# Optimization experiments

Measured on AMD Instinct MI355X. Metric: run time of the kernel, lower is better.

## Reference

```python
import jax, jax.numpy as jnp
import numpy as np

N_NODES = 100000
N_EDGES = 1600000
IN_F, HID, OUT_F = 50, 256, 121


def setup_inputs() -> dict:
    key = jax.random.key(0)
    ks = jax.random.split(key, 8)
    x = jax.random.normal(ks[0], (N_NODES, IN_F), dtype=jnp.float32)
    edge_index = jax.random.randint(ks[1], (2, N_EDGES), 0, N_NODES, dtype=jnp.int64)
    W1 = jax.random.normal(ks[2], (IN_F, HID), dtype=jnp.float32) * (1.0 / np.sqrt(IN_F))
    b1 = jnp.zeros((HID,), dtype=jnp.float32)
    W2 = jax.random.normal(ks[3], (HID, HID), dtype=jnp.float32) * (1.0 / np.sqrt(HID))
    b2 = jnp.zeros((HID,), dtype=jnp.float32)
    W3 = jax.random.normal(ks[4], (HID, OUT_F), dtype=jnp.float32) * (1.0 / np.sqrt(HID))
    b3 = jnp.zeros((OUT_F,), dtype=jnp.float32)
    return {"x": x, "edge_index": edge_index, "W1": W1, "b1": b1,
            "W2": W2, "b2": b2, "W3": W3, "b3": b3}


def _gcn_norm(edge_index, num_nodes):
    # PyG gcn_norm: add self-loops, symmetric degree normalization.
    loop = jnp.arange(num_nodes, dtype=edge_index.dtype)
    row = jnp.concatenate([edge_index[0], loop])  # source
    col = jnp.concatenate([edge_index[1], loop])  # target (aggregation dim)
    ones = jnp.ones(row.shape[0], dtype=jnp.float32)
    deg = jax.ops.segment_sum(ones, col, num_segments=num_nodes)
    dinv = jnp.where(deg > 0, jax.lax.rsqrt(deg), 0.0)
    norm = dinv[row] * dinv[col]  # [E+N]
    return row, col, norm


def _gcn_conv(x, W, b, row, col, norm, num_nodes):
    h = x @ W                                   # [N, F_out] dense transform
    msg = h[row] * norm[:, None]                # gather + scale  [E+N, F_out]
    agg = jax.ops.segment_sum(msg, col, num_segments=num_nodes)  # scatter-add
    return agg + b


def reference(x, edge_index, W1, b1, W2, b2, W3, b3):
    n = x.shape[0]
    row, col, norm = _gcn_norm(edge_index, n)
    # layer 1 + relu (dropout is identity in eval mode)
    x1 = _gcn_conv(x, W1, b1, row, col, norm, n)
    h = jax.nn.relu(x1)
    # layer 2 + relu
    x1 = _gcn_conv(h, W2, b2, row, col, norm, n)
    h = jax.nn.relu(x1)
    # layer 3; module returns pre-relu output x1 of the last conv
    x1 = _gcn_conv(h, W3, b3, row, col, norm, n)
    return x1
```

## Files before the change

### kernel.cpp

```cpp
#include <hip/hip_runtime.h>


#define IN_F 50
#define HID  256
#define OUT_F 121
#define KP1  64
#define NP3  128
#define MPAD 100096

typedef __attribute__((ext_vector_type(8))) short bf16x8;
typedef __attribute__((ext_vector_type(4))) float f32x4;

__device__ __forceinline__ float bf2f(unsigned short u) {
    union { unsigned int i; float f; } x; x.i = ((unsigned int)u) << 16; return x.f;
}
__device__ __forceinline__ unsigned short f2bf(float f) {
    union { float f; unsigned int i; } x; x.f = f;
    unsigned int r = x.i + 0x7FFFu + ((x.i >> 16) & 1u);
    return (unsigned short)(r >> 16);
}

__device__ __forceinline__ void gl2lds16(const void* g, void* l) {
    __builtin_amdgcn_global_load_lds(
        (const __attribute__((address_space(1))) void*)g,
        (__attribute__((address_space(3))) void*)l, 16, 0, 0);
}

__global__ void k_detect(const int* __restrict__ ei, int* __restrict__ flag, int N) {
    int i = threadIdx.x;
    int lo = ei[2 * i], hi = ei[2 * i + 1];
    int bad = (hi != 0) || ((unsigned)lo >= (unsigned)N);
    unsigned long long m = __ballot(bad);
    if (threadIdx.x == 0) *flag = (m == 0ULL) ? 1 : 0;
}


__global__ void k_count(const int* __restrict__ ei, const int* __restrict__ flag,
                        int* __restrict__ cnt, int E, int N) {
    int t = blockIdx.x * blockDim.x + threadIdx.x;
    if (t >= E) return;
    int f = *flag;
    int c = f ? ei[2 * (E + t)] : ei[E + t];
    c = min(max(c, 0), N - 1);
    atomicAdd(&cnt[c], 1);
}

__global__ __launch_bounds__(1024) void k_scan(const int* __restrict__ cnt,
                                               int* __restrict__ offs,
                                               float* __restrict__ dinv, int n) {
    __shared__ int wsum[16];
    __shared__ int s_carry;
    int lane = threadIdx.x & 63, wid = threadIdx.x >> 6;
    if (threadIdx.x == 0) s_carry = 0;
    __syncthreads();
    for (int base = 0; base < n; base += 4096) {
        int i0 = base + (int)threadIdx.x * 4;
        int v0 = (i0 + 0 < n) ? cnt[i0 + 0] : 0;
        int v1 = (i0 + 1 < n) ? cnt[i0 + 1] : 0;
        int v2 = (i0 + 2 < n) ? cnt[i0 + 2] : 0;
        int v3 = (i0 + 3 < n) ? cnt[i0 + 3] : 0;
        int s1 = v0 + v1, s2 = s1 + v2, tsum = s2 + v3;
        int x = tsum;
        #pragma unroll
        for (int d = 1; d < 64; d <<= 1) {
            int y = __shfl_up(x, d, 64);
            if (lane >= d) x += y;
        }
        if (lane == 63) wsum[wid] = x;
        __syncthreads();
        int wpre = 0;
        #pragma unroll
        for (int j = 0; j < 16; j++) wpre += (j < wid) ? wsum[j] : 0;
        int carry = s_carry;
        int e0 = carry + wpre + x - tsum;
        if (i0 + 0 < n) { offs[i0+0]=e0;    dinv[i0+0]=rsqrtf((float)(v0+1)); }
        if (i0 + 1 < n) { offs[i0+1]=e0+v0; dinv[i0+1]=rsqrtf((float)(v1+1)); }
        if (i0 + 2 < n) { offs[i0+2]=e0+s1; dinv[i0+2]=rsqrtf((float)(v2+1)); }
        if (i0 + 3 < n) { offs[i0+3]=e0+s2; dinv[i0+3]=rsqrtf((float)(v3+1)); }
        __syncthreads();
        if (threadIdx.x == 1023) s_carry = carry + wpre + x;
        __syncthreads();
    }
    if (threadIdx.x == 0) offs[n] = s_carry;
}

__global__ void k_fill(const int* __restrict__ ei, const int* __restrict__ flag,
                       const int* __restrict__ offs,
                       int* __restrict__ fillc, int* __restrict__ rowidx, int E, int N) {
    int t = blockIdx.x * blockDim.x + threadIdx.x;
    if (t >= E) return;
    int f = *flag;
    int c = f ? ei[2 * (E + t)] : ei[E + t];
    int r = f ? ei[2 * t] : ei[t];
    c = min(max(c, 0), N - 1);
    r = min(max(r, 0), N - 1);
    int pos = offs[c] + atomicAdd(&fillc[c], 1);
    if ((unsigned)pos < (unsigned)E) rowidx[pos] = r;
}


__global__ void k_padx(const float* __restrict__ x, const float* __restrict__ dinv,
                       unsigned short* __restrict__ Xs, int N) {
    int idx = blockIdx.x * blockDim.x + threadIdx.x;
    if (idx >= N * KP1) return;
    int node = idx >> 6, k = idx & 63;
    Xs[idx] = (k < IN_F) ? f2bf(dinv[node] * x[node * IN_F + k]) : (unsigned short)0;
}

__global__ void k_tr(const float* __restrict__ W, unsigned short* __restrict__ Bt,
                     int K, int Nw, int Kp, int Np) {
    int idx = blockIdx.x * blockDim.x + threadIdx.x;
    if (idx >= Np * Kp) return;
    int nn = idx / Kp, k = idx - nn * Kp;
    Bt[idx] = (k < K && nn < Nw) ? f2bf(W[k * Nw + nn]) : (unsigned short)0;
}

__global__ __launch_bounds__(256) void k_gemm_lds(const unsigned short* __restrict__ A,
                                                  const unsigned short* __restrict__ Bt,
                                                  const float* __restrict__ dinv,
                                                  const float* __restrict__ bias,
                                                  unsigned short* __restrict__ C,
                                                  int K, int Nout,
                                                  int BIAS, int RELU, int SCALE) {
    __shared__ char lds[16384];
    const int tid = threadIdx.x;
    const int wid = tid >> 6, lane = tid & 63;
    const int wm = wid & 1, wn = wid >> 1;
    const int quad = lane >> 4, ml = lane & 15;
    const int m0 = blockIdx.x * 128;
    const int n0g = blockIdx.y * 128;

    f32x4 acc[4][4];
    #pragma unroll
    for (int a = 0; a < 4; a++)
        #pragma unroll
        for (int b = 0; b < 4; b++) acc[a][b] = (f32x4){0.f, 0.f, 0.f, 0.f};

    for (int kk = 0; kk < K; kk += 32) {
        #pragma unroll
        for (int r = 0; r < 2; r++) {
            int c = r * 256 + tid;
            int row = c >> 2, q = c & 3;
            gl2lds16(A  + (size_t)(m0  + row) * K + kk + q * 8, lds + c * 16);
            gl2lds16(Bt + (size_t)(n0g + row) * K + kk + q * 8, lds + 8192 + c * 16);
        }
        __syncthreads();
        bf16x8 af[4], bfv[4];
        #pragma unroll
        for (int mf = 0; mf < 4; mf++)
            af[mf] = *(const bf16x8*)(lds + ((wm * 64 + mf * 16 + ml) * 64 + quad * 16));
        #pragma unroll
        for (int nf = 0; nf < 4; nf++)
            bfv[nf] = *(const bf16x8*)(lds + 8192 + ((wn * 64 + nf * 16 + ml) * 64 + quad * 16));
        #pragma unroll
        for (int mf = 0; mf < 4; mf++)
            #pragma unroll
            for (int nf = 0; nf < 4; nf++)
                acc[mf][nf] = __builtin_amdgcn_mfma_f32_16x16x32_bf16(af[mf], bfv[nf], acc[mf][nf], 0, 0, 0);
        __syncthreads();
    }

    #pragma unroll
    for (int mf = 0; mf < 4; mf++) {
        int r0 = m0 + wm * 64 + mf * 16 + quad * 4;
        float dd[4] = {1.f, 1.f, 1.f, 1.f};
        if (SCALE) { dd[0]=dinv[r0]; dd[1]=dinv[r0+1]; dd[2]=dinv[r0+2]; dd[3]=dinv[r0+3]; }
        #pragma unroll
        for (int nf = 0; nf < 4; nf++) {
            int col = n0g + wn * 64 + nf * 16 + ml;
            float bb = BIAS ? bias[col] : 0.f;
            #pragma unroll
            for (int i = 0; i < 4; i++) {
                float v = acc[mf][nf][i] + bb;
                if (RELU) v = fmaxf(v, 0.f);
                v *= dd[i];
                C[(size_t)(r0 + i) * Nout + col] = f2bf(v);
            }
        }
    }
}


__device__ __forceinline__ int rclamp(int r, int N) { return min(max(r, 0), N - 1); }

__global__ void k_aggx(const unsigned short* __restrict__ Xs,
                       const int* __restrict__ offs, const int* __restrict__ rowidx,
                       const float* __restrict__ dinv, unsigned short* __restrict__ Y, int N) {
    int wid = threadIdx.x >> 6, lane = threadIdx.x & 63;
    int sub = lane >> 3, sl = lane & 7;
    int node = blockIdx.x * 32 + wid * 8 + sub;
    int nc = min(node, N - 1);
    int c = sl * 8;
    bf16x8 s = *(const bf16x8*)(Xs + (size_t)nc * KP1 + c);
    float a[8];
    #pragma unroll
    for (int k = 0; k < 8; k++) a[k] = bf2f((unsigned short)s[k]);
    int e = offs[nc], end = offs[nc + 1];
    if (node >= N) { e = 0; end = 0; }
    while (__any(e < end)) {
        int r[4]; float m[4];
        #pragma unroll
        for (int j = 0; j < 4; j++) {
            int idx = e + j;
            m[j] = (idx < end) ? 1.f : 0.f;
            idx = min(idx, end - 1); idx = max(idx, 0);
            r[j] = rclamp(rowidx[idx], N);
        }
        bf16x8 u[4];
        #pragma unroll
        for (int j = 0; j < 4; j++)
            u[j] = *(const bf16x8*)(Xs + (size_t)r[j] * KP1 + c);
        #pragma unroll
        for (int j = 0; j < 4; j++)
            #pragma unroll
            for (int k = 0; k < 8; k++)
                a[k] = fmaf(bf2f((unsigned short)u[j][k]), m[j], a[k]);
        e += 4;
    }
    if (node < N) {
        float dv = dinv[node];
        bf16x8 o;
        #pragma unroll
        for (int k = 0; k < 8; k++) o[k] = (short)f2bf(a[k] * dv);
        *(bf16x8*)(Y + (size_t)node * KP1 + c) = o;
    }
}

__global__ void k_agg256(const unsigned short* __restrict__ Hn,
                         const int* __restrict__ offs, const int* __restrict__ rowidx,
                         const float* __restrict__ dinv, unsigned short* __restrict__ Y, int N) {
    int wid = threadIdx.x >> 6, lane = threadIdx.x & 63;
    int sub = lane >> 5, sl = lane & 31;
    int node = blockIdx.x * 8 + wid * 2 + sub;
    int nc = min(node, N - 1);
    int c = sl * 8;
    bf16x8 s = *(const bf16x8*)(Hn + (size_t)nc * HID + c);
    float a[8];
    #pragma unroll
    for (int k = 0; k < 8; k++) a[k] = bf2f((unsigned short)s[k]);
    int e = offs[nc], end = offs[nc + 1];
    if (node >= N) { e = 0; end = 0; }
    while (__any(e < end)) {
        int r[4]; float m[4];
        #pragma unroll
        for (int j = 0; j < 4; j++) {
            int idx = e + j;
            m[j] = (idx < end) ? 1.f : 0.f;
            idx = min(idx, end - 1); idx = max(idx, 0);
            r[j] = rclamp(rowidx[idx], N);
        }
        bf16x8 u[4];
        #pragma unroll
        for (int j = 0; j < 4; j++)
            u[j] = *(const bf16x8*)(Hn + (size_t)r[j] * HID + c);
        #pragma unroll
        for (int j = 0; j < 4; j++)
            #pragma unroll
            for (int k = 0; k < 8; k++)
                a[k] = fmaf(bf2f((unsigned short)u[j][k]), m[j], a[k]);
        e += 4;
    }
    if (node < N) {
        float dv = dinv[node];
        bf16x8 o;
        #pragma unroll
        for (int k = 0; k < 8; k++) o[k] = (short)f2bf(a[k] * dv);
        *(bf16x8*)(Y + (size_t)node * HID + c) = o;
    }
}

__global__ void k_aggout(const unsigned short* __restrict__ G,
                         const int* __restrict__ offs, const int* __restrict__ rowidx,
                         const float* __restrict__ dinv, const float* __restrict__ bias,
                         float* __restrict__ out, int N) {
    int wid = threadIdx.x >> 6, lane = threadIdx.x & 63;
    int sub = lane >> 4, sl = lane & 15;
    int node = blockIdx.x * 16 + wid * 4 + sub;
    int nc = min(node, N - 1);
    int c = sl * 8;
    bf16x8 s = *(const bf16x8*)(G + (size_t)nc * NP3 + c);
    float a[8];
    #pragma unroll
    for (int k = 0; k < 8; k++) a[k] = bf2f((unsigned short)s[k]);
    int e = offs[nc], end = offs[nc + 1];
    if (node >= N) { e = 0; end = 0; }
    while (__any(e < end)) {
        int r[4]; float m[4];
        #pragma unroll
        for (int j = 0; j < 4; j++) {
            int idx = e + j;
            m[j] = (idx < end) ? 1.f : 0.f;
            idx = min(idx, end - 1); idx = max(idx, 0);
            r[j] = rclamp(rowidx[idx], N);
        }
        bf16x8 u[4];
        #pragma unroll
        for (int j = 0; j < 4; j++)
            u[j] = *(const bf16x8*)(G + (size_t)r[j] * NP3 + c);
        #pragma unroll
        for (int j = 0; j < 4; j++)
            #pragma unroll
            for (int k = 0; k < 8; k++)
                a[k] = fmaf(bf2f((unsigned short)u[j][k]), m[j], a[k]);
        e += 4;
    }
    if (node < N) {
        float dv = dinv[node];
        #pragma unroll
        for (int k = 0; k < 8; k++) {
            int col = c + k;
            if (col < OUT_F)
                out[(size_t)node * OUT_F + col] = fmaf(a[k], dv, bias[col]);
        }
    }
}


extern "C" void kernel_launch(void* const* d_in, const int* in_sizes, int n_in,
                              void* d_out, int out_size, void* d_ws, size_t ws_size,
                              hipStream_t stream) {
    const float* x  = (const float*)d_in[0];
    const int*   ei = (const int*)d_in[1];
    const float* W1 = (const float*)d_in[2];
    const float* b1 = (const float*)d_in[3];
    const float* W2 = (const float*)d_in[4];
    const float* b2 = (const float*)d_in[5];
    const float* W3 = (const float*)d_in[6];
    const float* b3 = (const float*)d_in[7];
    float* out = (float*)d_out;

    const int N = in_sizes[0] / IN_F;
    const int E = in_sizes[1] / 2;

    char* w = (char*)d_ws;
    size_t off = 0;
    auto alloc = [&](size_t bytes) -> char* {
        char* p = w + off;
        off += (bytes + 255) & ~(size_t)255;
        return p;
    };
    int*   cnt    = (int*)  alloc((size_t)N * 4);
    int*   offs   = (int*)  alloc((size_t)(N + 1) * 4);
    int*   fillc  = (int*)  alloc((size_t)N * 4);
    float* dinv   = (float*)alloc((size_t)MPAD * 4);
    int*   flag   = (int*)  alloc(256);
    int*   rowidx = (int*)  alloc((size_t)E * 4);
    unsigned short* Bt1 = (unsigned short*)alloc((size_t)HID * KP1 * 2);
    unsigned short* Bt2 = (unsigned short*)alloc((size_t)HID * HID * 2);
    unsigned short* Bt3 = (unsigned short*)alloc((size_t)NP3 * HID * 2);
    unsigned short* bufA = (unsigned short*)alloc((size_t)MPAD * HID * 2);
    unsigned short* bufB = (unsigned short*)alloc((size_t)MPAD * HID * 2);
    unsigned short* Xs  = bufA;
    unsigned short* Y1  = bufB;
    unsigned short* H1s = bufA;
    unsigned short* Y2  = bufB;
    unsigned short* H2  = bufA;
    unsigned short* G3  = bufB;

    hipMemsetAsync(cnt, 0, (size_t)N * 4, stream);
    hipMemsetAsync(fillc, 0, (size_t)N * 4, stream);
    hipMemsetAsync(rowidx, 0, (size_t)E * 4, stream);

    k_detect<<<1, 64, 0, stream>>>(ei, flag, N);
    k_count<<<(E + 255) / 256, 256, 0, stream>>>(ei, flag, cnt, E, N);
    k_scan<<<1, 1024, 0, stream>>>(cnt, offs, dinv, N);
    k_fill<<<(E + 255) / 256, 256, 0, stream>>>(ei, flag, offs, fillc, rowidx, E, N);

    k_padx<<<(N * KP1 + 255) / 256, 256, 0, stream>>>(x, dinv, Xs, N);
    k_tr<<<(HID * KP1 + 255) / 256, 256, 0, stream>>>(W1, Bt1, IN_F, HID, KP1, HID);
    k_tr<<<(HID * HID + 255) / 256, 256, 0, stream>>>(W2, Bt2, HID, HID, HID, HID);
    k_tr<<<(NP3 * HID + 255) / 256, 256, 0, stream>>>(W3, Bt3, HID, OUT_F, HID, NP3);

    dim3 g12(MPAD / 128, HID / 128);
    dim3 g3(MPAD / 128, NP3 / 128);

    k_aggx<<<(N + 31) / 32, 256, 0, stream>>>(Xs, offs, rowidx, dinv, Y1, N);
    k_gemm_lds<<<g12, 256, 0, stream>>>(Y1, Bt1, dinv, b1, H1s, KP1, HID, 1, 1, 1);
    k_agg256<<<(N + 7) / 8, 256, 0, stream>>>(H1s, offs, rowidx, dinv, Y2, N);
    k_gemm_lds<<<g12, 256, 0, stream>>>(Y2, Bt2, dinv, b2, H2, HID, HID, 1, 1, 0);
    k_gemm_lds<<<g3, 256, 0, stream>>>(H2, Bt3, dinv, b3, G3, HID, NP3, 0, 0, 1);
    k_aggout<<<(N + 15) / 16, 256, 0, stream>>>(G3, offs, rowidx, dinv, b3, out, N);

    (void)n_in; (void)out_size; (void)ws_size;
}
```

Measured before the change: 662.2 us.

## Fuse neighbor aggregation with the dense GEMM for GCN layers one and two

Replaces the separate aggregate-then-GEMM kernel pairs for layers 1 and 2 with a single kernel. Each wave gathers and sums neighbor rows directly into MFMA A-fragment registers, then multiplies them by weight tiles streamed through LDS. This removes the Y1/Y2 intermediate writes and reads and two launches. The cost is one edge per loop iteration instead of four, which gives less memory-level parallelism. Layer 2 also needs large per-lane register arrays (K32=8 gives 64 floats of accumulator), so occupancy may drop and per-block gather divergence grows.

```diff
diff --git a/kernel.cpp b/kernel.cpp
--- a/kernel.cpp
+++ b/kernel.cpp
@@ -115,6 +115,98 @@
     Bt[idx] = (k < K && nn < Nw) ? f2bf(W[k * Nw + nn]) : (unsigned short)0;
 }
 
+__device__ __forceinline__ int rclamp(int r, int N) { return min(max(r, 0), N - 1); }
+
+template<int K32, int SCALE>
+__global__ __launch_bounds__(256) void k_fused(const unsigned short* __restrict__ Hsrc,
+                                               const unsigned short* __restrict__ Bt,
+                                               const int* __restrict__ offs,
+                                               const int* __restrict__ rowidx,
+                                               const float* __restrict__ dinv,
+                                               const float* __restrict__ bias,
+                                               unsigned short* __restrict__ Cout,
+                                               int N) {
+    __shared__ char lds[16384];
+    const int K = K32 * 32;
+    const int tid = threadIdx.x;
+    const int wid = tid >> 6, lane = tid & 63;
+    const int quad = lane >> 4, ml = lane & 15;
+    const int g = blockIdx.x * 64 + wid * 16 + ml;
+    const int gc = min(g, N - 1);
+
+    float accA[K32][8];
+    {
+        #pragma unroll
+        for (int ks = 0; ks < K32; ks++) {
+            bf16x8 v = *(const bf16x8*)(Hsrc + (size_t)gc * K + ks * 32 + quad * 8);
+            #pragma unroll
+            for (int j = 0; j < 8; j++) accA[ks][j] = bf2f((unsigned short)v[j]);
+        }
+    }
+    int e = offs[gc], end = offs[gc + 1];
+    if (g >= N) { e = 0; end = 0; }
+    while (__any(e < end)) {
+        int ec = min(e, max(end - 1, 0));
+        int src = rclamp(rowidx[ec], N);
+        float m = (e < end) ? 1.0f : 0.0f;
+        bf16x8 u[K32];
+        #pragma unroll
+        for (int ks = 0; ks < K32; ks++)
+            u[ks] = *(const bf16x8*)(Hsrc + (size_t)src * K + ks * 32 + quad * 8);
+        #pragma unroll
+        for (int ks = 0; ks < K32; ks++)
+            #pragma unroll
+            for (int j = 0; j < 8; j++)
+                accA[ks][j] = fmaf(bf2f((unsigned short)u[ks][j]), m, accA[ks][j]);
+        e++;
+    }
+    float dv = dinv[gc];
+    bf16x8 af[K32];
+    #pragma unroll
+    for (int ks = 0; ks < K32; ks++)
+        #pragma unroll
+        for (int j = 0; j < 8; j++) af[ks][j] = (short)f2bf(accA[ks][j] * dv);
+
+    f32x4 accC[16];
+    #pragma unroll
+    for (int nf = 0; nf < 16; nf++) accC[nf] = (f32x4){0.f, 0.f, 0.f, 0.f};
+
+    for (int ks = 0; ks < K32; ks++) {
+        __syncthreads();
+        #pragma unroll
+        for (int i = 0; i < 4; i++) {
+            int c = i * 256 + tid;
+            int nn = c >> 2, q = c & 3;
+            gl2lds16(Bt + (size_t)nn * K + ks * 32 + q * 8, lds + c * 16);
+        }
+        __syncthreads();
+        bf16x8 a;
+        #pragma unroll
+        for (int s = 0; s < K32; s++) if (s == ks) a = af[s];
+        #pragma unroll
+        for (int nf = 0; nf < 16; nf++) {
+            bf16x8 bfv = *(const bf16x8*)(lds + ((nf * 16 + ml) * 64 + quad * 16));
+            accC[nf] = __builtin_amdgcn_mfma_f32_16x16x32_bf16(a, bfv, accC[nf], 0, 0, 0);
+        }
+    }
+
+    int r0 = blockIdx.x * 64 + wid * 16 + quad * 4;
+    float dd[4] = {1.f, 1.f, 1.f, 1.f};
+    if (SCALE) { dd[0]=dinv[r0]; dd[1]=dinv[r0+1]; dd[2]=dinv[r0+2]; dd[3]=dinv[r0+3]; }
+    #pragma unroll
+    for (int nf = 0; nf < 16; nf++) {
+        int col = nf * 16 + ml;
+        float bb = bias[col];
+        #pragma unroll
+        for (int i = 0; i < 4; i++) {
+            float v = accC[nf][i] + bb;
+            v = fmaxf(v, 0.f);
+            v *= dd[i];
+            Cout[(size_t)(r0 + i) * HID + col] = f2bf(v);
+        }
+    }
+}
+
 __global__ __launch_bounds__(256) void k_gemm_lds(const unsigned short* __restrict__ A,
                                                   const unsigned short* __restrict__ Bt,
                                                   const float* __restrict__ dinv,
@@ -177,95 +269,6 @@
                 C[(size_t)(r0 + i) * Nout + col] = f2bf(v);
             }
         }
-    }
-}
-
-
-__device__ __forceinline__ int rclamp(int r, int N) { return min(max(r, 0), N - 1); }
-
-__global__ void k_aggx(const unsigned short* __restrict__ Xs,
-                       const int* __restrict__ offs, const int* __restrict__ rowidx,
-                       const float* __restrict__ dinv, unsigned short* __restrict__ Y, int N) {
-    int wid = threadIdx.x >> 6, lane = threadIdx.x & 63;
-    int sub = lane >> 3, sl = lane & 7;
-    int node = blockIdx.x * 32 + wid * 8 + sub;
-    int nc = min(node, N - 1);
-    int c = sl * 8;
-    bf16x8 s = *(const bf16x8*)(Xs + (size_t)nc * KP1 + c);
-    float a[8];
-    #pragma unroll
-    for (int k = 0; k < 8; k++) a[k] = bf2f((unsigned short)s[k]);
-    int e = offs[nc], end = offs[nc + 1];
-    if (node >= N) { e = 0; end = 0; }
-    while (__any(e < end)) {
-        int r[4]; float m[4];
-        #pragma unroll
-        for (int j = 0; j < 4; j++) {
-            int idx = e + j;
-            m[j] = (idx < end) ? 1.f : 0.f;
-            idx = min(idx, end - 1); idx = max(idx, 0);
-            r[j] = rclamp(rowidx[idx], N);
-        }
-        bf16x8 u[4];
-        #pragma unroll
-        for (int j = 0; j < 4; j++)
-            u[j] = *(const bf16x8*)(Xs + (size_t)r[j] * KP1 + c);
-        #pragma unroll
-        for (int j = 0; j < 4; j++)
-            #pragma unroll
-            for (int k = 0; k < 8; k++)
-                a[k] = fmaf(bf2f((unsigned short)u[j][k]), m[j], a[k]);
-        e += 4;
-    }
-    if (node < N) {
-        float dv = dinv[node];
-        bf16x8 o;
-        #pragma unroll
-        for (int k = 0; k < 8; k++) o[k] = (short)f2bf(a[k] * dv);
-        *(bf16x8*)(Y + (size_t)node * KP1 + c) = o;
-    }
-}
-
-__global__ void k_agg256(const unsigned short* __restrict__ Hn,
-                         const int* __restrict__ offs, const int* __restrict__ rowidx,
-                         const float* __restrict__ dinv, unsigned short* __restrict__ Y, int N) {
-    int wid = threadIdx.x >> 6, lane = threadIdx.x & 63;
-    int sub = lane >> 5, sl = lane & 31;
-    int node = blockIdx.x * 8 + wid * 2 + sub;
-    int nc = min(node, N - 1);
-    int c = sl * 8;
-    bf16x8 s = *(const bf16x8*)(Hn + (size_t)nc * HID + c);
-    float a[8];
-    #pragma unroll
-    for (int k = 0; k < 8; k++) a[k] = bf2f((unsigned short)s[k]);
-    int e = offs[nc], end = offs[nc + 1];
-    if (node >= N) { e = 0; end = 0; }
-    while (__any(e < end)) {
-        int r[4]; float m[4];
-        #pragma unroll
-        for (int j = 0; j < 4; j++) {
-            int idx = e + j;
-            m[j] = (idx < end) ? 1.f : 0.f;
-            idx = min(idx, end - 1); idx = max(idx, 0);
-            r[j] = rclamp(rowidx[idx], N);
-        }
-        bf16x8 u[4];
-        #pragma unroll
-        for (int j = 0; j < 4; j++)
-            u[j] = *(const bf16x8*)(Hn + (size_t)r[j] * HID + c);
-        #pragma unroll
-        for (int j = 0; j < 4; j++)
-            #pragma unroll
-            for (int k = 0; k < 8; k++)
-                a[k] = fmaf(bf2f((unsigned short)u[j][k]), m[j], a[k]);
-        e += 4;
-    }
-    if (node < N) {
-        float dv = dinv[node];
-        bf16x8 o;
-        #pragma unroll
-        for (int k = 0; k < 8; k++) o[k] = (short)f2bf(a[k] * dv);
-        *(bf16x8*)(Y + (size_t)node * HID + c) = o;
     }
 }
 
@@ -351,9 +354,7 @@
     unsigned short* bufA = (unsigned short*)alloc((size_t)MPAD * HID * 2);
     unsigned short* bufB = (unsigned short*)alloc((size_t)MPAD * HID * 2);
     unsigned short* Xs  = bufA;
-    unsigned short* Y1  = bufB;
-    unsigned short* H1s = bufA;
-    unsigned short* Y2  = bufB;
+    unsigned short* H1s = bufB;
     unsigned short* H2  = bufA;
     unsigned short* G3  = bufB;
 
@@ -371,13 +372,10 @@
     k_tr<<<(HID * HID + 255) / 256, 256, 0, stream>>>(W2, Bt2, HID, HID, HID, HID);
     k_tr<<<(NP3 * HID + 255) / 256, 256, 0, stream>>>(W3, Bt3, HID, OUT_F, HID, NP3);
 
-    dim3 g12(MPAD / 128, HID / 128);
+    const int fgrid = MPAD / 64;
+    k_fused<2, 1><<<fgrid, 256, 0, stream>>>(Xs, Bt1, offs, rowidx, dinv, b1, H1s, N);
+    k_fused<8, 0><<<fgrid, 256, 0, stream>>>(H1s, Bt2, offs, rowidx, dinv, b2, H2, N);
     dim3 g3(MPAD / 128, NP3 / 128);
-
-    k_aggx<<<(N + 31) / 32, 256, 0, stream>>>(Xs, offs, rowidx, dinv, Y1, N);
-    k_gemm_lds<<<g12, 256, 0, stream>>>(Y1, Bt1, dinv, b1, H1s, KP1, HID, 1, 1, 1);
-    k_agg256<<<(N + 7) / 8, 256, 0, stream>>>(H1s, offs, rowidx, dinv, Y2, N);
-    k_gemm_lds<<<g12, 256, 0, stream>>>(Y2, Bt2, dinv, b2, H2, HID, HID, 1, 1, 0);
     k_gemm_lds<<<g3, 256, 0, stream>>>(H2, Bt3, dinv, b3, G3, HID, NP3, 0, 0, 1);
     k_aggout<<<(N + 15) / 16, 256, 0, stream>>>(G3, offs, rowidx, dinv, b3, out, N);
 
```

New measurement: 827.0 us. 1.25x slower.

## Split aggregation kernels into feature-column chunks with 8-way block interleaving

Applied to the files above, without the earlier changes.

The 256-wide and output aggregation kernels now give each 8-lane group one node and only a 64-column chunk of features. Block IDs are interleaved so that the 8 blocks sharing an index cover different column chunks and node ranges (halves or quarters). Each gathered row slice is 128 bytes, so the working set of concurrently running blocks is narrower and more of it may stay in L2/MALL during the random gathers. In exchange, the edge index lists are read once per chunk, and there are more, shorter wavefronts per node.

```diff
diff --git a/kernel.cpp b/kernel.cpp
--- a/kernel.cpp
+++ b/kernel.cpp
@@ -226,28 +226,34 @@
     }
 }
 
-__global__ void k_agg256(const unsigned short* __restrict__ Hn,
-                         const int* __restrict__ offs, const int* __restrict__ rowidx,
-                         const float* __restrict__ dinv, unsigned short* __restrict__ Y, int N) {
+__global__ void k_agg256s(const unsigned short* __restrict__ Hn,
+                          const int* __restrict__ offs, const int* __restrict__ rowidx,
+                          const float* __restrict__ dinv, unsigned short* __restrict__ Y,
+                          int N, int half_n) {
+    int cell = blockIdx.x & 7;
+    int chunk = cell >> 1, half = cell & 1;
+    int idx = blockIdx.x >> 3;
     int wid = threadIdx.x >> 6, lane = threadIdx.x & 63;
-    int sub = lane >> 5, sl = lane & 31;
-    int node = blockIdx.x * 8 + wid * 2 + sub;
-    int nc = min(node, N - 1);
-    int c = sl * 8;
+    int sub = lane >> 3, sl = lane & 7;
+    int node = half * half_n + idx * 32 + wid * 8 + sub;
+    int hi_end = min((half + 1) * half_n, N);
+    int ok = node < hi_end;
+    int nc = ok ? node : hi_end - 1;
+    int c = chunk * 64 + sl * 8;
     bf16x8 s = *(const bf16x8*)(Hn + (size_t)nc * HID + c);
     float a[8];
     #pragma unroll
     for (int k = 0; k < 8; k++) a[k] = bf2f((unsigned short)s[k]);
     int e = offs[nc], end = offs[nc + 1];
-    if (node >= N) { e = 0; end = 0; }
+    if (!ok) { e = 0; end = 0; }
     while (__any(e < end)) {
         int r[4]; float m[4];
         #pragma unroll
         for (int j = 0; j < 4; j++) {
-            int idx = e + j;
-            m[j] = (idx < end) ? 1.f : 0.f;
-            idx = min(idx, end - 1); idx = max(idx, 0);
-            r[j] = rclamp(rowidx[idx], N);
+            int idx2 = e + j;
+            m[j] = (idx2 < end) ? 1.f : 0.f;
+            idx2 = min(idx2, end - 1); idx2 = max(idx2, 0);
+            r[j] = rclamp(rowidx[idx2], N);
         }
         bf16x8 u[4];
         #pragma unroll
@@ -260,7 +266,7 @@
                 a[k] = fmaf(bf2f((unsigned short)u[j][k]), m[j], a[k]);
         e += 4;
     }
-    if (node < N) {
+    if (ok) {
         float dv = dinv[node];
         bf16x8 o;
         #pragma unroll
@@ -269,29 +275,34 @@
     }
 }
 
-__global__ void k_aggout(const unsigned short* __restrict__ G,
-                         const int* __restrict__ offs, const int* __restrict__ rowidx,
-                         const float* __restrict__ dinv, const float* __restrict__ bias,
-                         float* __restrict__ out, int N) {
+__global__ void k_aggouts(const unsigned short* __restrict__ G,
+                          const int* __restrict__ offs, const int* __restrict__ rowidx,
+                          const float* __restrict__ dinv, const float* __restrict__ bias,
+                          float* __restrict__ out, int N, int quar_n) {
+    int cell = blockIdx.x & 7;
+    int chunk = cell >> 2, quar = cell & 3;
+    int idx = blockIdx.x >> 3;
     int wid = threadIdx.x >> 6, lane = threadIdx.x & 63;
-    int sub = lane >> 4, sl = lane & 15;
-    int node = blockIdx.x * 16 + wid * 4 + sub;
-    int nc = min(node, N - 1);
-    int c = sl * 8;
+    int sub = lane >> 3, sl = lane & 7;
+    int node = quar * quar_n + idx * 32 + wid * 8 + sub;
+    int hi_end = min((quar + 1) * quar_n, N);
+    int ok = node < hi_end;
+    int nc = ok ? node : hi_end - 1;
+    int c = chunk * 64 + sl * 8;
     bf16x8 s = *(const bf16x8*)(G + (size_t)nc * NP3 + c);
     float a[8];
     #pragma unroll
     for (int k = 0; k < 8; k++) a[k] = bf2f((unsigned short)s[k]);
     int e = offs[nc], end = offs[nc + 1];
-    if (node >= N) { e = 0; end = 0; }
+    if (!ok) { e = 0; end = 0; }
     while (__any(e < end)) {
         int r[4]; float m[4];
         #pragma unroll
         for (int j = 0; j < 4; j++) {
-            int idx = e + j;
-            m[j] = (idx < end) ? 1.f : 0.f;
-            idx = min(idx, end - 1); idx = max(idx, 0);
-            r[j] = rclamp(rowidx[idx], N);
+            int idx2 = e + j;
+            m[j] = (idx2 < end) ? 1.f : 0.f;
+            idx2 = min(idx2, end - 1); idx2 = max(idx2, 0);
+            r[j] = rclamp(rowidx[idx2], N);
         }
         bf16x8 u[4];
         #pragma unroll
@@ -304,7 +315,7 @@
                 a[k] = fmaf(bf2f((unsigned short)u[j][k]), m[j], a[k]);
         e += 4;
     }
-    if (node < N) {
+    if (ok) {
         float dv = dinv[node];
         #pragma unroll
         for (int k = 0; k < 8; k++) {
@@ -374,12 +385,17 @@
     dim3 g12(MPAD / 128, HID / 128);
     dim3 g3(MPAD / 128, NP3 / 128);
 
+    int half_n = (N + 1) / 2;
+    int bpc2 = (half_n + 31) / 32;
+    int quar_n = (N + 3) / 4;
+    int bpc3 = (quar_n + 31) / 32;
+
     k_aggx<<<(N + 31) / 32, 256, 0, stream>>>(Xs, offs, rowidx, dinv, Y1, N);
     k_gemm_lds<<<g12, 256, 0, stream>>>(Y1, Bt1, dinv, b1, H1s, KP1, HID, 1, 1, 1);
-    k_agg256<<<(N + 7) / 8, 256, 0, stream>>>(H1s, offs, rowidx, dinv, Y2, N);
+    k_agg256s<<<8 * bpc2, 256, 0, stream>>>(H1s, offs, rowidx, dinv, Y2, N, half_n);
     k_gemm_lds<<<g12, 256, 0, stream>>>(Y2, Bt2, dinv, b2, H2, HID, HID, 1, 1, 0);
     k_gemm_lds<<<g3, 256, 0, stream>>>(H2, Bt3, dinv, b3, G3, HID, NP3, 0, 0, 1);
-    k_aggout<<<(N + 15) / 16, 256, 0, stream>>>(G3, offs, rowidx, dinv, b3, out, N);
+    k_aggouts<<<8 * bpc3, 256, 0, stream>>>(G3, offs, rowidx, dinv, b3, out, N, quar_n);
 
     (void)n_in; (void)out_size; (void)ws_size;
 }
```

New measurement: 639.3 us. 1.04x faster.
